# Optimization experiments

Measured on AMD Instinct MI355X. Metric: run time of the kernel, lower is better.

The kernel has to match this reference:

```python
import jax, jax.numpy as jnp
import numpy as np
from jax import lax

T, LC = 4096, 20           # sentence length, max word length in chars
CV, CE, CO = 100, 25, 25   # char vocab, char emb dim, char-cnn out channels
V, E = 100000, 512         # word vocab, word emb dim
H = 1024                   # lstm hidden size per direction
NT, START, STOP = 12, 10, 11
NEG = -10000.0


def _lstm_dir(x, w_ih, w_hh, b_ih, b_hh):
    # x: [T, In] -> hs: [T, H]; pytorch gate order i, f, g, o
    pre = x @ w_ih.T + (b_ih + b_hh)              # [T, 4H] (input part hoisted out of scan)
    h0 = jnp.zeros((H,), x.dtype)
    def step(carry, p):
        h, c = carry
        g = p + h @ w_hh.T
        i, f, gg, o = jnp.split(g, 4)
        i = jax.nn.sigmoid(i); f = jax.nn.sigmoid(f)
        gg = jnp.tanh(gg); o = jax.nn.sigmoid(o)
        c = f * c + i * gg
        h = o * jnp.tanh(c)
        return (h, c), h
    _, hs = lax.scan(step, (h0, h0), pre)
    return hs


def _features(sentence, chars, char_emb, cnn_w, cnn_b, word_emb,
              w_ih_f, w_hh_f, b_ih_f, b_hh_f, w_ih_b, w_hh_b, b_ih_b, b_hh_b,
              w_tag, b_tag):
    # char CNN: embed -> conv2d(kernel (3,CE), pad (2,0)) -> max-pool over full time axis
    ce = char_emb[chars][:, None, :, :]            # [T,1,LC,CE]
    y = lax.conv_general_dilated(ce, cnn_w, (1, 1), ((2, 2), (0, 0)),
                                 dimension_numbers=('NCHW', 'OIHW', 'NCHW'))
    y = y + cnn_b[None, :, None, None]             # [T,CO,LC+2,1]
    char_feat = y.max(axis=(2, 3))                 # [T,CO]
    emb = jnp.concatenate([word_emb[sentence], char_feat], axis=1)  # [T,E+CO]
    # dropout is identity in eval mode
    hf = _lstm_dir(emb, w_ih_f, w_hh_f, b_ih_f, b_hh_f)
    hb = _lstm_dir(emb[::-1], w_ih_b, w_hh_b, b_ih_b, b_hh_b)[::-1]
    out = jnp.concatenate([hf, hb], axis=1)        # [T,2H]
    return out @ w_tag.T + b_tag                   # [T,NT]


def _viterbi(feats, transitions):
    alpha0 = jnp.full((NT,), NEG, feats.dtype).at[START].set(0.0)
    def step(alpha, feat):
        smat = alpha[:, None] + feat[None, :] + transitions   # [from, to]
        return jax.nn.logsumexp(smat, axis=0), jnp.argmax(smat, axis=0)
    alpha, bptrs = lax.scan(step, alpha0, feats)               # bptrs: [T,NT]
    final = alpha + transitions[:, STOP]                       # [NT]
    score = jax.nn.logsumexp(final)
    best_last = jnp.argmax(final)
    def back(best, b):
        nb = b[best]
        return nb, nb
    _, prev = lax.scan(back, best_last, bptrs[1:][::-1])
    path = jnp.concatenate([prev[::-1], best_last[None]])      # [T]
    return score, path


def setup_inputs() -> dict:
    key = jax.random.key(0)
    ks = jax.random.split(key, 18)
    IN = E + CO
    tr = jax.random.normal(ks[17], (NT, NT), jnp.float32)
    tr = tr.at[:, START].set(NEG).at[STOP, :].set(NEG)
    return {
        'sentence': jax.random.randint(ks[0], (T,), 0, V),
        'chars': jax.random.randint(ks[1], (T, LC), 0, CV),
        'caps': jax.random.randint(ks[2], (T,), 0, 4),
        'char_emb': jax.random.normal(ks[3], (CV, CE), jnp.float32),
        'cnn_w': jax.random.normal(ks[4], (CO, 1, 3, CE), jnp.float32) * 0.1,
        'cnn_b': jax.random.normal(ks[5], (CO,), jnp.float32) * 0.1,
        'word_emb': jax.random.normal(ks[6], (V, E), jnp.float32),
        'w_ih_f': jax.random.normal(ks[7], (4 * H, IN), jnp.float32) * 0.02,
        'w_hh_f': jax.random.normal(ks[8], (4 * H, H), jnp.float32) * 0.02,
        'b_ih_f': jax.random.normal(ks[9], (4 * H,), jnp.float32) * 0.02,
        'b_hh_f': jax.random.normal(ks[10], (4 * H,), jnp.float32) * 0.02,
        'w_ih_b': jax.random.normal(ks[11], (4 * H, IN), jnp.float32) * 0.02,
        'w_hh_b': jax.random.normal(ks[12], (4 * H, H), jnp.float32) * 0.02,
        'b_ih_b': jax.random.normal(ks[13], (4 * H,), jnp.float32) * 0.02,
        'b_hh_b': jax.random.normal(ks[14], (4 * H,), jnp.float32) * 0.02,
        'w_tag': jax.random.normal(ks[15], (NT, 2 * H), jnp.float32) * 0.02,
        'b_tag': jax.random.normal(ks[16], (NT,), jnp.float32) * 0.02,
        'transitions': tr,
    }


def reference(sentence, chars, caps, char_emb, cnn_w, cnn_b, word_emb,
              w_ih_f, w_hh_f, b_ih_f, b_hh_f, w_ih_b, w_hh_b, b_ih_b, b_hh_b,
              w_tag, b_tag, transitions):
    # caps is accepted by the original forward signature but never used
    feats = _features(sentence, chars, char_emb, cnn_w, cnn_b, word_emb,
                      w_ih_f, w_hh_f, b_ih_f, b_hh_f, w_ih_b, w_hh_b,
                      b_ih_b, b_hh_b, w_tag, b_tag)
    return _viterbi(feats, transitions)
```

## Files before the change

kernel.cpp:

```cpp
#include <hip/hip_runtime.h>
#include <math.h>


#define T_LEN 4096
#define NTAG 12
#define START_TAG 10
#define STOP_TAG 11
#define NEG_VAL (-10000.0f)

typedef int   v4i __attribute__((ext_vector_type(4)));
typedef float v4f __attribute__((ext_vector_type(4)));

#define OF_EMB  0UL
#define OF_W    (OF_EMB + 4096UL * 544UL)
#define OF_BIAS (OF_W + 8192UL * 544UL)
#define OF_PRE  (OF_BIAS + 8192UL)
#define OF_HF   (OF_PRE + 4096UL * 8192UL)
#define OF_HB   (OF_HF + 4097UL * 1024UL)
#define OF_FEAT (OF_HB + 4097UL * 1024UL)

__device__ __forceinline__ float fsig(float v) {
    return 1.0f / (1.0f + __expf(-v));
}
__device__ __forceinline__ float ftanhf(float v) {
    float a = fabsf(v);
    float e = __expf(-2.0f * a);
    float r = (1.0f - e) / (1.0f + e);
    return copysignf(r, v);
}

__global__ void prep_w_kernel(const float* __restrict__ wf, const float* __restrict__ wb,
                              const float* __restrict__ bif, const float* __restrict__ bhf,
                              const float* __restrict__ bib, const float* __restrict__ bhb,
                              float* __restrict__ wpad, float* __restrict__ bias) {
    int n = blockIdx.x;
    const float* src = (n < 4096) ? (wf + (size_t)n * 537) : (wb + (size_t)(n - 4096) * 537);
    float* dst = wpad + (size_t)n * 544;
    for (int k = threadIdx.x; k < 544; k += blockDim.x)
        dst[k] = (k < 537) ? src[k] : 0.f;
    if (threadIdx.x == 0)
        bias[n] = (n < 4096) ? (bif[n] + bhf[n]) : (bib[n - 4096] + bhb[n - 4096]);
}

__global__ void charcnn_kernel(const int* __restrict__ sentence, const int* __restrict__ chars,
                               const float* __restrict__ cemb, const float* __restrict__ cw,
                               const float* __restrict__ cb, const float* __restrict__ wemb,
                               float* __restrict__ emb) {
    int t = blockIdx.x, tid = threadIdx.x;
    __shared__ float ce[500];
    __shared__ float yv[550];
    for (int i = tid; i < 500; i += 256) {
        int c = chars[t * 20 + i / 25];
        ce[i] = cemb[c * 25 + i % 25];
    }
    __syncthreads();
    for (int i = tid; i < 550; i += 256) {
        int o = i / 22, p = i % 22;
        float v = cb[o];
        #pragma unroll
        for (int kh = 0; kh < 3; ++kh) {
            int ir = p - 2 + kh;
            if (ir >= 0 && ir < 20) {
                const float* crow = ce + ir * 25;
                const float* wrow = cw + o * 75 + kh * 25;
                #pragma unroll
                for (int kw = 0; kw < 25; ++kw) v = fmaf(crow[kw], wrow[kw], v);
            }
        }
        yv[o * 22 + p] = v;
    }
    __syncthreads();
    float* erow = emb + (size_t)t * 544;
    int sidx = sentence[t];
    if (tid < 128)
        ((float4*)erow)[tid] = ((const float4*)(wemb + (size_t)sidx * 512))[tid];
    if (tid >= 128 && tid < 153) {
        int o = tid - 128;
        const float* yo = yv + o * 22;
        float m = yo[0];
        #pragma unroll
        for (int p = 1; p < 22; ++p) m = fmaxf(m, yo[p]);
        erow[512 + o] = m;
    }
    if (tid >= 160 && tid < 167) erow[537 + (tid - 160)] = 0.f;
}

__global__ __launch_bounds__(256) void sgemm_kernel(const float* __restrict__ A,
                                                    const float* __restrict__ B,
                                                    const float* __restrict__ bias,
                                                    float* __restrict__ C) {
    __shared__ float As[8 * 128];
    __shared__ float Bs[8 * 128];
    const int tid = threadIdx.x;
    const int tx = tid & 15, ty = tid >> 4;
    const int t0 = blockIdx.y * 128, n0 = blockIdx.x * 128;
    const int r = tid >> 1, cq = tid & 1;
    const int rsw = r ^ (((r >> 5) & 3) << 2);
    float acc[8][8];
    #pragma unroll
    for (int i = 0; i < 8; ++i)
        #pragma unroll
        for (int j = 0; j < 8; ++j) acc[i][j] = 0.f;
    const float* Ap = A + (size_t)(t0 + r) * 544 + cq * 4;
    const float* Bp = B + (size_t)(n0 + r) * 544 + cq * 4;
    const int bsw = ((tx >> 2) & 3) << 2;
    for (int kt = 0; kt < 68; ++kt) {
        float4 av = *(const float4*)(Ap + kt * 8);
        float4 bv = *(const float4*)(Bp + kt * 8);
        __syncthreads();
        As[(cq * 4 + 0) * 128 + r] = av.x;
        As[(cq * 4 + 1) * 128 + r] = av.y;
        As[(cq * 4 + 2) * 128 + r] = av.z;
        As[(cq * 4 + 3) * 128 + r] = av.w;
        Bs[(cq * 4 + 0) * 128 + rsw] = bv.x;
        Bs[(cq * 4 + 1) * 128 + rsw] = bv.y;
        Bs[(cq * 4 + 2) * 128 + rsw] = bv.z;
        Bs[(cq * 4 + 3) * 128 + rsw] = bv.w;
        __syncthreads();
        #pragma unroll
        for (int k = 0; k < 8; ++k) {
            float a[8], b[8];
            #pragma unroll
            for (int i = 0; i < 8; ++i) a[i] = As[k * 128 + ty * 8 + i];
            #pragma unroll
            for (int j = 0; j < 8; ++j) b[j] = Bs[k * 128 + ((tx * 8 + j) ^ bsw)];
            #pragma unroll
            for (int i = 0; i < 8; ++i)
                #pragma unroll
                for (int j = 0; j < 8; ++j) acc[i][j] = fmaf(a[i], b[j], acc[i][j]);
        }
    }
    float bz[8];
    #pragma unroll
    for (int j = 0; j < 8; ++j) bz[j] = bias[n0 + tx * 8 + j];
    #pragma unroll
    for (int i = 0; i < 8; ++i) {
        float* crow = C + (size_t)(t0 + ty * 8 + i) * 8192 + n0 + tx * 8;
        float4 s0 = make_float4(acc[i][0] + bz[0], acc[i][1] + bz[1], acc[i][2] + bz[2], acc[i][3] + bz[3]);
        float4 s1 = make_float4(acc[i][4] + bz[4], acc[i][5] + bz[5], acc[i][6] + bz[6], acc[i][7] + bz[7]);
        ((float4*)crow)[0] = s0;
        ((float4*)crow)[1] = s1;
    }
}

__global__ __launch_bounds__(512, 2) void lstm_kernel(const float* __restrict__ whhf,
                                                      const float* __restrict__ whhb,
                                                      const float* __restrict__ pre,
                                                      float* __restrict__ hfbuf,
                                                      float* __restrict__ hbbuf) {
    const int tid = threadIdx.x;
    const int dir = blockIdx.x >> 6;
    const int widx = blockIdx.x & 63;
    const int j0 = widx * 16;
    const int c32 = tid >> 4;
    const int r4 = tid & 15;
    const int lane = tid & 63;
    const int wv = tid >> 6;
    const bool pol = (r4 < 8);
    __shared__ __align__(16) float partials[2][8][64];

    float4 w[4][8];
    #pragma unroll
    for (int i = 0; i < 4; ++i) {
        int R = 4 * r4 + i;
        const float4* ws = (const float4*)((dir ? whhb : whhf) +
            (size_t)(((R >> 4) << 10) + j0 + (R & 15)) * 1024 + c32 * 32);
        #pragma unroll
        for (int m = 0; m < 8; ++m) w[i][m] = ws[m];
    }

    float* hbuf = dir ? hbbuf : hfbuf;
    const int dirofs = dir ? 4096 : 0;
    float c = 0.f;

    for (int s = 0; s < T_LEN; ++s) {
        const int t = dir ? (T_LEN - 1 - s) : s;
        const int rdslot = dir ? (t + 1) : t;
        const int wrslot = dir ? t : (t + 1);
        const int p = s & 1;

        float preg = 0.f;
        if (tid < 64)
            preg = pre[(size_t)t * 8192 + dirofs + ((lane & 3) << 10) + j0 + (lane >> 2)];

        const float* hp = hbuf + ((size_t)rdslot << 10) + c32 * 32 + r4 * 4;
        v4i hq;
        hq.x = 0; hq.y = 0; hq.z = 0; hq.w = 0;
        if (pol) {
            asm volatile("global_load_dwordx4 %0, %1, off sc1\n\ts_waitcnt vmcnt(0)"
                         : "=v"(hq) : "v"(hp));
        }
        while (true) {
            bool miss = pol && (hq.x == -1 || hq.y == -1 || hq.z == -1 || hq.w == -1);
            if (!__any(miss)) break;
            __builtin_amdgcn_s_sleep(1);
            if (miss) {
                asm volatile("global_load_dwordx4 %0, %1, off sc1\n\ts_waitcnt vmcnt(0)"
                             : "=v"(hq) : "v"(hp));
            }
        }

        float a0 = 0.f, a1 = 0.f, a2 = 0.f, a3 = 0.f;
        #pragma unroll
        for (int m = 0; m < 8; ++m) {
            int src = (lane & 48) + m;
            float hx = __shfl(__int_as_float(hq.x), src);
            float hy = __shfl(__int_as_float(hq.y), src);
            float hz = __shfl(__int_as_float(hq.z), src);
            float hw = __shfl(__int_as_float(hq.w), src);
            a0 = fmaf(w[0][m].x, hx, a0); a0 = fmaf(w[0][m].y, hy, a0);
            a0 = fmaf(w[0][m].z, hz, a0); a0 = fmaf(w[0][m].w, hw, a0);
            a1 = fmaf(w[1][m].x, hx, a1); a1 = fmaf(w[1][m].y, hy, a1);
            a1 = fmaf(w[1][m].z, hz, a1); a1 = fmaf(w[1][m].w, hw, a1);
            a2 = fmaf(w[2][m].x, hx, a2); a2 = fmaf(w[2][m].y, hy, a2);
            a2 = fmaf(w[2][m].z, hz, a2); a2 = fmaf(w[2][m].w, hw, a2);
            a3 = fmaf(w[3][m].x, hx, a3); a3 = fmaf(w[3][m].y, hy, a3);
            a3 = fmaf(w[3][m].z, hz, a3); a3 = fmaf(w[3][m].w, hw, a3);
        }
        a0 += __shfl_xor(a0, 16); a0 += __shfl_xor(a0, 32);
        a1 += __shfl_xor(a1, 16); a1 += __shfl_xor(a1, 32);
        a2 += __shfl_xor(a2, 16); a2 += __shfl_xor(a2, 32);
        a3 += __shfl_xor(a3, 16); a3 += __shfl_xor(a3, 32);
        if ((lane >> 4) == 0)
            *(float4*)&partials[p][wv][r4 << 2] = make_float4(a0, a1, a2, a3);
        __syncthreads();

        if (tid < 64) {
            int rql = ((lane & 3) << 4) + (lane >> 2);
            float dsum = 0.f;
            #pragma unroll
            for (int q = 0; q < 8; ++q) dsum += partials[p][q][rql];
            float val = preg + dsum;
            float act = ((lane & 3) == 2) ? ftanhf(val) : fsig(val);
            int base = lane & ~3;
            float iv = __shfl(act, base);
            float fv = __shfl(act, base + 1);
            float gv = __shfl(act, base + 2);
            float ov = __shfl(act, base + 3);
            c = fv * c + iv * gv;
            float h = ov * ftanhf(c);
            v4f hv;
            hv.x = __shfl(h, (lane << 4) & 63);
            hv.y = __shfl(h, ((lane << 4) + 4) & 63);
            hv.z = __shfl(h, ((lane << 4) + 8) & 63);
            hv.w = __shfl(h, ((lane << 4) + 12) & 63);
            if (lane < 4) {
                float* hp2 = hbuf + ((size_t)wrslot << 10) + j0 + (lane << 2);
                asm volatile("global_store_dwordx4 %0, %1, off sc1"
                             :: "v"(hp2), "v"(hv));
            }
        }
    }
}

__global__ __launch_bounds__(192) void tagproj_kernel(const float* __restrict__ hfbuf,
                                                      const float* __restrict__ hbbuf,
                                                      const float* __restrict__ wtag,
                                                      const float* __restrict__ btag,
                                                      float* __restrict__ feats) {
    int t = blockIdx.x, tid = threadIdx.x;
    __shared__ float4 hs4[512];
    for (int i = tid; i < 512; i += 192) {
        float4 q = (i < 256)
            ? ((const float4*)(hfbuf + ((size_t)(t + 1) << 10)))[i]
            : ((const float4*)(hbbuf + ((size_t)t << 10)))[i - 256];
        hs4[i ^ ((i >> 5) & 7)] = q;
    }
    __syncthreads();
    int tag = tid >> 4, sl = tid & 15;
    const float4* wrow4 = (const float4*)(wtag + (size_t)tag * 2048 + (sl << 7));
    float a = 0.f;
    #pragma unroll
    for (int m = 0; m < 32; ++m) {
        float4 h4 = hs4[(sl << 5) + (m ^ (sl & 7))];
        float4 w4 = wrow4[m];
        a = fmaf(h4.x, w4.x, a);
        a = fmaf(h4.y, w4.y, a);
        a = fmaf(h4.z, w4.z, a);
        a = fmaf(h4.w, w4.w, a);
    }
    a += __shfl_xor(a, 1);
    a += __shfl_xor(a, 2);
    a += __shfl_xor(a, 4);
    a += __shfl_xor(a, 8);
    if (sl == 0) feats[t * 12 + tag] = a + btag[tag];
}

__global__ __launch_bounds__(64) void viterbi_kernel(const float* __restrict__ feats,
                                                     const float* __restrict__ trans,
                                                     float* __restrict__ out) {
    const int tid = threadIdx.x;
    __shared__ float fbuf[256 * 12];
    __shared__ unsigned char bp[4096 * 12];
    __shared__ __align__(16) float alph[12];
    __shared__ __align__(16) float finv[12];
    float trf[12];
    float tstop = 0.f;
    if (tid < 12) {
        #pragma unroll
        for (int f = 0; f < 12; ++f) trf[f] = trans[f * 12 + tid];
        tstop = trans[tid * 12 + STOP_TAG];
        alph[tid] = (tid == START_TAG) ? 0.f : NEG_VAL;
    }
    __syncthreads();
    for (int ck = 0; ck < 16; ++ck) {
        for (int i = tid; i < 3072; i += 64) fbuf[i] = feats[ck * 3072 + i];
        __syncthreads();
        for (int tt = 0; tt < 256; ++tt) {
            if (tid < 12) {
                float feat = fbuf[tt * 12 + tid];
                float4 A0 = *(const float4*)(alph);
                float4 A1 = *(const float4*)(alph + 4);
                float4 A2 = *(const float4*)(alph + 8);
                float av[12] = {A0.x, A0.y, A0.z, A0.w, A1.x, A1.y, A1.z, A1.w,
                                A2.x, A2.y, A2.z, A2.w};
                float sv[12];
                float m = -INFINITY;
                int best = 0;
                #pragma unroll
                for (int f = 0; f < 12; ++f) {
                    float s2 = (av[f] + feat) + trf[f];
                    sv[f] = s2;
                    if (s2 > m) { m = s2; best = f; }
                }
                float sum = 0.f;
                #pragma unroll
                for (int f = 0; f < 12; ++f) sum += __expf(sv[f] - m);
                bp[(ck * 256 + tt) * 12 + tid] = (unsigned char)best;
                alph[tid] = __logf(sum) + m;
            }
            __syncthreads();
        }
    }
    if (tid < 12) finv[tid] = alph[tid] + tstop;
    __syncthreads();
    if (tid < 12) {
        float4 F0 = *(const float4*)(finv);
        float4 F1 = *(const float4*)(finv + 4);
        float4 F2 = *(const float4*)(finv + 8);
        float fv[12] = {F0.x, F0.y, F0.z, F0.w, F1.x, F1.y, F1.z, F1.w,
                        F2.x, F2.y, F2.z, F2.w};
        float m = -INFINITY;
        int bl = 0;
        #pragma unroll
        for (int f = 0; f < 12; ++f)
            if (fv[f] > m) { m = fv[f]; bl = f; }
        float sum = 0.f;
        #pragma unroll
        for (int f = 0; f < 12; ++f) sum += __expf(fv[f] - m);
        float score = __logf(sum) + m;
        if (tid == 0) {
            out[0] = score;
            out[4096] = (float)bl;
        }
        int cur = bl;
        for (int tt = 4095; tt >= 1; --tt) {
            int bv = (int)bp[tt * 12 + tid];
            cur = __shfl(bv, cur);
            if (tid == 0) out[tt] = (float)cur;
        }
    }
}

extern "C" void kernel_launch(void* const* d_in, const int* in_sizes, int n_in,
                              void* d_out, int out_size, void* d_ws, size_t ws_size,
                              hipStream_t stream) {
    (void)in_sizes; (void)n_in; (void)out_size; (void)ws_size;
    const int* sentence = (const int*)d_in[0];
    const int* chars = (const int*)d_in[1];
    const float* cemb = (const float*)d_in[3];
    const float* cw = (const float*)d_in[4];
    const float* cb = (const float*)d_in[5];
    const float* wemb = (const float*)d_in[6];
    const float* w_ih_f = (const float*)d_in[7];
    const float* w_hh_f = (const float*)d_in[8];
    const float* b_ih_f = (const float*)d_in[9];
    const float* b_hh_f = (const float*)d_in[10];
    const float* w_ih_b = (const float*)d_in[11];
    const float* w_hh_b = (const float*)d_in[12];
    const float* b_ih_b = (const float*)d_in[13];
    const float* b_hh_b = (const float*)d_in[14];
    const float* wtag = (const float*)d_in[15];
    const float* btag = (const float*)d_in[16];
    const float* trans = (const float*)d_in[17];

    float* ws = (float*)d_ws;
    float* emb = ws + OF_EMB;
    float* wpad = ws + OF_W;
    float* bias = ws + OF_BIAS;
    float* pre = ws + OF_PRE;
    float* hf = ws + OF_HF;
    float* hb = ws + OF_HB;
    float* feats = ws + OF_FEAT;

    (void)hipMemsetAsync(hf, 0xFF, 4097UL * 1024UL * 4UL, stream);
    (void)hipMemsetAsync(hb, 0xFF, 4097UL * 1024UL * 4UL, stream);
    (void)hipMemsetAsync(hf, 0x00, 1024UL * 4UL, stream);
    (void)hipMemsetAsync(hb + 4096UL * 1024UL, 0x00, 1024UL * 4UL, stream);

    hipLaunchKernelGGL(prep_w_kernel, dim3(8192), dim3(256), 0, stream,
                       w_ih_f, w_ih_b, b_ih_f, b_hh_f, b_ih_b, b_hh_b, wpad, bias);
    hipLaunchKernelGGL(charcnn_kernel, dim3(4096), dim3(256), 0, stream,
                       sentence, chars, cemb, cw, cb, wemb, emb);
    hipLaunchKernelGGL(sgemm_kernel, dim3(64, 32), dim3(256), 0, stream,
                       emb, wpad, bias, pre);
    hipLaunchKernelGGL(lstm_kernel, dim3(128), dim3(512), 0, stream,
                       w_hh_f, w_hh_b, pre, hf, hb);
    hipLaunchKernelGGL(tagproj_kernel, dim3(4096), dim3(192), 0, stream,
                       hf, hb, wtag, btag, feats);
    hipLaunchKernelGGL(viterbi_kernel, dim3(1), dim3(64), 0, stream,
                       feats, trans, (float*)d_out);
}
```

Baseline: 11.56 ms.

## Split LSTM recurrence across 256 workgroups with 8 hidden units each

The persistent LSTM kernel now uses 128 workgroups per direction instead of 64, each owning 8 hidden units (32 gate rows) rather than 16. Each thread holds 64 recurrent weights in registers instead of 128, and computes one gate-row partial sum, so the per-step dot product and the cross-lane reduction both shrink. Per-step compute is spread over more CUs, at the cost of more workgroups polling the shared h buffer and more global synchronization traffic each timestep. Launch bounds are raised so the lighter register footprint fits the higher occupancy target.

```diff
diff --git a/kernel.cpp b/kernel.cpp
--- a/kernel.cpp
+++ b/kernel.cpp
@@ -7,6 +7,7 @@
 #define START_TAG 10
 #define STOP_TAG 11
 #define NEG_VAL (-10000.0f)
+#define NWGD 128
 
 typedef int   v4i __attribute__((ext_vector_type(4)));
 typedef float v4f __attribute__((ext_vector_type(4)));
@@ -143,30 +144,30 @@
     }
 }
 
-__global__ __launch_bounds__(512, 2) void lstm_kernel(const float* __restrict__ whhf,
+__global__ __launch_bounds__(512, 4) void lstm_kernel(const float* __restrict__ whhf,
                                                       const float* __restrict__ whhb,
                                                       const float* __restrict__ pre,
                                                       float* __restrict__ hfbuf,
                                                       float* __restrict__ hbbuf) {
     const int tid = threadIdx.x;
-    const int dir = blockIdx.x >> 6;
-    const int widx = blockIdx.x & 63;
-    const int j0 = widx * 16;
-    const int c32 = tid >> 4;
-    const int r4 = tid & 15;
+    const int dir = blockIdx.x >> 7;
+    const int widx = blockIdx.x & 127;
+    const int j0 = widx * 8;
+    const int R = tid & 31;
+    const int cgrp = tid >> 5;
     const int lane = tid & 63;
     const int wv = tid >> 6;
-    const bool pol = (r4 < 8);
-    __shared__ __align__(16) float partials[2][8][64];
-
-    float4 w[4][8];
-    #pragma unroll
-    for (int i = 0; i < 4; ++i) {
-        int R = 4 * r4 + i;
-        const float4* ws = (const float4*)((dir ? whhb : whhf) +
-            (size_t)(((R >> 4) << 10) + j0 + (R & 15)) * 1024 + c32 * 32);
-        #pragma unroll
-        for (int m = 0; m < 8; ++m) w[i][m] = ws[m];
+    const bool pol = (lane < 32);
+    __shared__ __align__(16) float partials[2][8][32];
+
+    v4f w[16];
+    {
+        const v4f* wsrc = (const v4f*)((dir ? whhb : whhf) +
+            (size_t)(((R >> 3) << 10) + j0 + (R & 7)) * 1024 + (cgrp << 6));
+        #pragma unroll
+        for (int m = 0; m < 16; ++m) w[m] = wsrc[m];
+        #pragma unroll
+        for (int m = 0; m < 16; ++m) asm volatile("" : "+v"(w[m]));
     }
 
     float* hbuf = dir ? hbbuf : hfbuf;
@@ -180,10 +181,10 @@
         const int p = s & 1;
 
         float preg = 0.f;
-        if (tid < 64)
-            preg = pre[(size_t)t * 8192 + dirofs + ((lane & 3) << 10) + j0 + (lane >> 2)];
-
-        const float* hp = hbuf + ((size_t)rdslot << 10) + c32 * 32 + r4 * 4;
+        if (tid < 32)
+            preg = pre[(size_t)t * 8192 + dirofs + ((tid >> 3) << 10) + j0 + (tid & 7)];
+
+        const float* hp = hbuf + ((size_t)rdslot << 10) + (wv << 7) + (lane << 2);
         v4i hq;
         hq.x = 0; hq.y = 0; hq.z = 0; hq.w = 0;
         if (pol) {
@@ -200,52 +201,44 @@
             }
         }
 
-        float a0 = 0.f, a1 = 0.f, a2 = 0.f, a3 = 0.f;
-        #pragma unroll
-        for (int m = 0; m < 8; ++m) {
-            int src = (lane & 48) + m;
+        const int sbase = (lane & 32) >> 1;
+        float acc = 0.f;
+        #pragma unroll
+        for (int k = 0; k < 16; ++k) {
+            int src = sbase + k;
             float hx = __shfl(__int_as_float(hq.x), src);
             float hy = __shfl(__int_as_float(hq.y), src);
             float hz = __shfl(__int_as_float(hq.z), src);
             float hw = __shfl(__int_as_float(hq.w), src);
-            a0 = fmaf(w[0][m].x, hx, a0); a0 = fmaf(w[0][m].y, hy, a0);
-            a0 = fmaf(w[0][m].z, hz, a0); a0 = fmaf(w[0][m].w, hw, a0);
-            a1 = fmaf(w[1][m].x, hx, a1); a1 = fmaf(w[1][m].y, hy, a1);
-            a1 = fmaf(w[1][m].z, hz, a1); a1 = fmaf(w[1][m].w, hw, a1);
-            a2 = fmaf(w[2][m].x, hx, a2); a2 = fmaf(w[2][m].y, hy, a2);
-            a2 = fmaf(w[2][m].z, hz, a2); a2 = fmaf(w[2][m].w, hw, a2);
-            a3 = fmaf(w[3][m].x, hx, a3); a3 = fmaf(w[3][m].y, hy, a3);
-            a3 = fmaf(w[3][m].z, hz, a3); a3 = fmaf(w[3][m].w, hw, a3);
-        }
-        a0 += __shfl_xor(a0, 16); a0 += __shfl_xor(a0, 32);
-        a1 += __shfl_xor(a1, 16); a1 += __shfl_xor(a1, 32);
-        a2 += __shfl_xor(a2, 16); a2 += __shfl_xor(a2, 32);
-        a3 += __shfl_xor(a3, 16); a3 += __shfl_xor(a3, 32);
-        if ((lane >> 4) == 0)
-            *(float4*)&partials[p][wv][r4 << 2] = make_float4(a0, a1, a2, a3);
+            acc = fmaf(w[k].x, hx, acc);
+            acc = fmaf(w[k].y, hy, acc);
+            acc = fmaf(w[k].z, hz, acc);
+            acc = fmaf(w[k].w, hw, acc);
+        }
+        acc += __shfl_xor(acc, 32);
+        if (pol) partials[p][wv][lane] = acc;
         __syncthreads();
 
-        if (tid < 64) {
-            int rql = ((lane & 3) << 4) + (lane >> 2);
+        if (tid < 32) {
             float dsum = 0.f;
             #pragma unroll
-            for (int q = 0; q < 8; ++q) dsum += partials[p][q][rql];
+            for (int q = 0; q < 8; ++q) dsum += partials[p][q][tid];
             float val = preg + dsum;
-            float act = ((lane & 3) == 2) ? ftanhf(val) : fsig(val);
-            int base = lane & ~3;
-            float iv = __shfl(act, base);
-            float fv = __shfl(act, base + 1);
-            float gv = __shfl(act, base + 2);
-            float ov = __shfl(act, base + 3);
+            float act = ((tid >> 3) == 2) ? ftanhf(val) : fsig(val);
+            int u = tid & 7;
+            float iv = __shfl(act, u);
+            float fv = __shfl(act, 8 + u);
+            float gv = __shfl(act, 16 + u);
+            float ov = __shfl(act, 24 + u);
             c = fv * c + iv * gv;
             float h = ov * ftanhf(c);
             v4f hv;
-            hv.x = __shfl(h, (lane << 4) & 63);
-            hv.y = __shfl(h, ((lane << 4) + 4) & 63);
-            hv.z = __shfl(h, ((lane << 4) + 8) & 63);
-            hv.w = __shfl(h, ((lane << 4) + 12) & 63);
-            if (lane < 4) {
-                float* hp2 = hbuf + ((size_t)wrslot << 10) + j0 + (lane << 2);
+            hv.x = __shfl(h, ((tid << 2) + 0) & 63);
+            hv.y = __shfl(h, ((tid << 2) + 1) & 63);
+            hv.z = __shfl(h, ((tid << 2) + 2) & 63);
+            hv.w = __shfl(h, ((tid << 2) + 3) & 63);
+            if (tid < 2) {
+                float* hp2 = hbuf + ((size_t)wrslot << 10) + j0 + (tid << 2);
                 asm volatile("global_store_dwordx4 %0, %1, off sc1"
                              :: "v"(hp2), "v"(hv));
             }
@@ -404,7 +397,7 @@
                        sentence, chars, cemb, cw, cb, wemb, emb);
     hipLaunchKernelGGL(sgemm_kernel, dim3(64, 32), dim3(256), 0, stream,
                        emb, wpad, bias, pre);
-    hipLaunchKernelGGL(lstm_kernel, dim3(128), dim3(512), 0, stream,
+    hipLaunchKernelGGL(lstm_kernel, dim3(256), dim3(512), 0, stream,
                        w_hh_f, w_hh_b, pre, hf, hb);
     hipLaunchKernelGGL(tagproj_kernel, dim3(4096), dim3(192), 0, stream,
                        hf, hb, wtag, btag, feats);
```

Result: slower. 15.02 ms (+29.9%).

## Stream bf16-packed recurrent weights from memory each LSTM step instead of registers

Applied to the files above, without the earlier changes.

Adds a prep kernel that converts the hidden-to-hidden LSTM weights to bf16 and packs them into a per-thread interleaved layout, reusing the embedding workspace region. The recurrent kernel no longer holds fp32 weights in registers. It reloads 16 packed uint4 values per thread from global memory/L2 on every timestep and unpacks them for the FMAs. This cuts register pressure and halves weight bytes, but puts a weight load on the serial critical path of each step and loses precision in the recurrent matmul.

```diff
diff --git a/kernel.cpp b/kernel.cpp
--- a/kernel.cpp
+++ b/kernel.cpp
@@ -28,6 +28,13 @@
     float r = (1.0f - e) / (1.0f + e);
     return copysignf(r, v);
 }
+__device__ __forceinline__ unsigned f2bf(float x) {
+    unsigned u = __float_as_uint(x);
+    u += 0x7fffu + ((u >> 16) & 1u);
+    return u >> 16;
+}
+__device__ __forceinline__ float bflo(unsigned d) { return __uint_as_float(d << 16); }
+__device__ __forceinline__ float bfhi(unsigned d) { return __uint_as_float(d & 0xffff0000u); }
 
 __global__ void prep_w_kernel(const float* __restrict__ wf, const float* __restrict__ wb,
                               const float* __restrict__ bif, const float* __restrict__ bhf,
@@ -40,6 +47,28 @@
         dst[k] = (k < 537) ? src[k] : 0.f;
     if (threadIdx.x == 0)
         bias[n] = (n < 4096) ? (bif[n] + bhf[n]) : (bib[n - 4096] + bhb[n - 4096]);
+}
+
+__global__ __launch_bounds__(512) void prep_whh_kernel(const float* __restrict__ wf,
+                                                       const float* __restrict__ wb,
+                                                       uint4* __restrict__ wpk4) {
+    int b = blockIdx.x, tid = threadIdx.x;
+    int dir = b >> 6, widx = b & 63;
+    int r4 = tid & 15, c32 = tid >> 4;
+    const float* W = dir ? wb : wf;
+    int j0 = widx * 16;
+    #pragma unroll
+    for (int q = 0; q < 16; ++q) {
+        int i = q >> 2;
+        int R = 4 * r4 + i;
+        const float* row = W + (size_t)(((R >> 4) << 10) + j0 + (R & 15)) * 1024
+                           + c32 * 32 + (q & 3) * 8;
+        unsigned d0 = (f2bf(row[1]) << 16) | f2bf(row[0]);
+        unsigned d1 = (f2bf(row[3]) << 16) | f2bf(row[2]);
+        unsigned d2 = (f2bf(row[5]) << 16) | f2bf(row[4]);
+        unsigned d3 = (f2bf(row[7]) << 16) | f2bf(row[6]);
+        wpk4[((size_t)b * 16 + q) * 512 + tid] = make_uint4(d0, d1, d2, d3);
+    }
 }
 
 __global__ void charcnn_kernel(const int* __restrict__ sentence, const int* __restrict__ chars,
@@ -143,8 +172,7 @@
     }
 }
 
-__global__ __launch_bounds__(512, 2) void lstm_kernel(const float* __restrict__ whhf,
-                                                      const float* __restrict__ whhb,
+__global__ __launch_bounds__(512, 2) void lstm_kernel(const uint4* __restrict__ wpk4,
                                                       const float* __restrict__ pre,
                                                       float* __restrict__ hfbuf,
                                                       float* __restrict__ hbbuf) {
@@ -159,16 +187,7 @@
     const bool pol = (r4 < 8);
     __shared__ __align__(16) float partials[2][8][64];
 
-    float4 w[4][8];
-    #pragma unroll
-    for (int i = 0; i < 4; ++i) {
-        int R = 4 * r4 + i;
-        const float4* ws = (const float4*)((dir ? whhb : whhf) +
-            (size_t)(((R >> 4) << 10) + j0 + (R & 15)) * 1024 + c32 * 32);
-        #pragma unroll
-        for (int m = 0; m < 8; ++m) w[i][m] = ws[m];
-    }
-
+    const uint4* wq = wpk4 + (size_t)(dir * 64 + widx) * 16 * 512 + tid;
     float* hbuf = dir ? hbbuf : hfbuf;
     const int dirofs = dir ? 4096 : 0;
     float c = 0.f;
@@ -178,6 +197,12 @@
         const int rdslot = dir ? (t + 1) : t;
         const int wrslot = dir ? t : (t + 1);
         const int p = s & 1;
+
+        v4i wd[16];
+        #pragma unroll
+        for (int q = 0; q < 16; ++q)
+            asm volatile("global_load_dwordx4 %0, %1, off"
+                         : "=v"(wd[q]) : "v"(wq + q * 512));
 
         float preg = 0.f;
         if (tid < 64)
@@ -208,14 +233,22 @@
             float hy = __shfl(__int_as_float(hq.y), src);
             float hz = __shfl(__int_as_float(hq.z), src);
             float hw = __shfl(__int_as_float(hq.w), src);
-            a0 = fmaf(w[0][m].x, hx, a0); a0 = fmaf(w[0][m].y, hy, a0);
-            a0 = fmaf(w[0][m].z, hz, a0); a0 = fmaf(w[0][m].w, hw, a0);
-            a1 = fmaf(w[1][m].x, hx, a1); a1 = fmaf(w[1][m].y, hy, a1);
-            a1 = fmaf(w[1][m].z, hz, a1); a1 = fmaf(w[1][m].w, hw, a1);
-            a2 = fmaf(w[2][m].x, hx, a2); a2 = fmaf(w[2][m].y, hy, a2);
-            a2 = fmaf(w[2][m].z, hz, a2); a2 = fmaf(w[2][m].w, hw, a2);
-            a3 = fmaf(w[3][m].x, hx, a3); a3 = fmaf(w[3][m].y, hy, a3);
-            a3 = fmaf(w[3][m].z, hz, a3); a3 = fmaf(w[3][m].w, hw, a3);
+            unsigned d00 = (m & 1) ? (unsigned)wd[0 + (m >> 1)].z : (unsigned)wd[0 + (m >> 1)].x;
+            unsigned d01 = (m & 1) ? (unsigned)wd[0 + (m >> 1)].w : (unsigned)wd[0 + (m >> 1)].y;
+            unsigned d10 = (m & 1) ? (unsigned)wd[4 + (m >> 1)].z : (unsigned)wd[4 + (m >> 1)].x;
+            unsigned d11 = (m & 1) ? (unsigned)wd[4 + (m >> 1)].w : (unsigned)wd[4 + (m >> 1)].y;
+            unsigned d20 = (m & 1) ? (unsigned)wd[8 + (m >> 1)].z : (unsigned)wd[8 + (m >> 1)].x;
+            unsigned d21 = (m & 1) ? (unsigned)wd[8 + (m >> 1)].w : (unsigned)wd[8 + (m >> 1)].y;
+            unsigned d30 = (m & 1) ? (unsigned)wd[12 + (m >> 1)].z : (unsigned)wd[12 + (m >> 1)].x;
+            unsigned d31 = (m & 1) ? (unsigned)wd[12 + (m >> 1)].w : (unsigned)wd[12 + (m >> 1)].y;
+            a0 = fmaf(bflo(d00), hx, a0); a0 = fmaf(bfhi(d00), hy, a0);
+            a0 = fmaf(bflo(d01), hz, a0); a0 = fmaf(bfhi(d01), hw, a0);
+            a1 = fmaf(bflo(d10), hx, a1); a1 = fmaf(bfhi(d10), hy, a1);
+            a1 = fmaf(bflo(d11), hz, a1); a1 = fmaf(bfhi(d11), hw, a1);
+            a2 = fmaf(bflo(d20), hx, a2); a2 = fmaf(bfhi(d20), hy, a2);
+            a2 = fmaf(bflo(d21), hz, a2); a2 = fmaf(bfhi(d21), hw, a2);
+            a3 = fmaf(bflo(d30), hx, a3); a3 = fmaf(bfhi(d30), hy, a3);
+            a3 = fmaf(bflo(d31), hz, a3); a3 = fmaf(bfhi(d31), hw, a3);
         }
         a0 += __shfl_xor(a0, 16); a0 += __shfl_xor(a0, 32);
         a1 += __shfl_xor(a1, 16); a1 += __shfl_xor(a1, 32);
@@ -392,6 +425,7 @@
     float* hf = ws + OF_HF;
     float* hb = ws + OF_HB;
     float* feats = ws + OF_FEAT;
+    uint4* wpk4 = (uint4*)(ws + OF_EMB);
 
     (void)hipMemsetAsync(hf, 0xFF, 4097UL * 1024UL * 4UL, stream);
     (void)hipMemsetAsync(hb, 0xFF, 4097UL * 1024UL * 4UL, stream);
@@ -404,8 +438,10 @@
                        sentence, chars, cemb, cw, cb, wemb, emb);
     hipLaunchKernelGGL(sgemm_kernel, dim3(64, 32), dim3(256), 0, stream,
                        emb, wpad, bias, pre);
+    hipLaunchKernelGGL(prep_whh_kernel, dim3(128), dim3(512), 0, stream,
+                       w_hh_f, w_hh_b, wpk4);
     hipLaunchKernelGGL(lstm_kernel, dim3(128), dim3(512), 0, stream,
-                       w_hh_f, w_hh_b, pre, hf, hb);
+                       wpk4, pre, hf, hb);
     hipLaunchKernelGGL(tagproj_kernel, dim3(4096), dim3(192), 0, stream,
                        hf, hb, wtag, btag, feats);
     hipLaunchKernelGGL(viterbi_kernel, dim3(1), dim3(64), 0, stream,
```

Result: slower. 14.61 ms (+26.4%).
